# Kernel optimization log

Hardware: AMD Instinct MI355X
Metric: run time of the kernel (lower is better)

Reference implementation:

```python
import jax, jax.numpy as jnp
import numpy as np

EPS = 1e-5


def _interp_conv(x, pos_in, pos_out, idx, w1, b1, w2, b2, kernel, bias):
    # x: [B, Cin, Nin]; idx: [Nout, K] neighbor indices into the input grid.
    off = pos_in[idx] - pos_out[:, None, :]            # [Nout, K, 2] relative offsets
    h = jax.nn.relu(off @ w1 + b1)                     # [Nout, K, 16] weight-net hidden
    A = h @ w2 + b2                                    # [Nout, K, T] interp weights onto T kernel taps
    feat = x[:, :, idx]                                # [B, Cin, Nout, K] irregular gather
    taps = jnp.einsum('bcnk,nkt->bcnt', feat, A)       # resample neighbors onto canonical taps
    return jnp.einsum('bcnt,oct->bon', taps, kernel) + bias[None, :, None]


def _bn_relu(x, g, b):
    # BatchNorm1d (training-style batch stats over (B, N)) + ReLU
    m = x.mean(axis=(0, 2), keepdims=True)
    v = x.var(axis=(0, 2), keepdims=True)
    return jax.nn.relu((x - m) * jax.lax.rsqrt(v + EPS) * g[None, :, None] + b[None, :, None])


def setup_inputs():
    key = jax.random.key(0)
    ks = jax.random.split(key, 24)
    B, N1, N2, N3, K, T = 16, 50176, 12544, 3136, 9, 9
    d = {}
    d['x'] = jax.random.normal(ks[0], (B, 3, N1), jnp.float32)
    d['l1'] = jax.random.uniform(ks[1], (N1, 2), jnp.float32)
    d['l2'] = jax.random.uniform(ks[2], (N2, 2), jnp.float32)
    d['l3'] = jax.random.uniform(ks[3], (N3, 2), jnp.float32)
    d['knn1'] = jax.random.randint(ks[4], (N2, K), 0, N1)
    d['knn2'] = jax.random.randint(ks[5], (N2, K), 0, N2)
    d['knn3'] = jax.random.randint(ks[6], (N2, K), 0, N2)
    d['pool_idx'] = jax.random.randint(ks[7], (N3, 4), 0, N2)
    cins = {'c1': 3, 'c2': 32, 'c3': 32}
    couts = {'c1': 32, 'c2': 32, 'c3': 64}
    for i, p in enumerate(['c1', 'c2', 'c3']):
        d[p + '_wn_w1'] = jax.random.normal(ks[8 + 4 * i], (2, 16), jnp.float32) * 0.5
        d[p + '_wn_b1'] = jnp.zeros(16, jnp.float32)
        d[p + '_wn_w2'] = jax.random.normal(ks[9 + 4 * i], (16, T), jnp.float32) * 0.3
        d[p + '_wn_b2'] = jnp.zeros(T, jnp.float32)
        d[p + '_kernel'] = jax.random.normal(ks[10 + 4 * i], (couts[p], cins[p], T), jnp.float32) * np.float32(1.0 / np.sqrt(cins[p] * T))
        d[p + '_bias'] = jnp.zeros(couts[p], jnp.float32)
    for p, c in [('bn1', 32), ('bn2', 32), ('bn3', 64)]:
        d[p + '_g'] = jnp.ones(c, jnp.float32)
        d[p + '_b'] = jnp.zeros(c, jnp.float32)
    return d


def reference(x, l1, l2, l3, knn1, knn2, knn3, pool_idx,
              c1_wn_w1, c1_wn_b1, c1_wn_w2, c1_wn_b2, c1_kernel, c1_bias,
              c2_wn_w1, c2_wn_b1, c2_wn_w2, c2_wn_b2, c2_kernel, c2_bias,
              c3_wn_w1, c3_wn_b1, c3_wn_w2, c3_wn_b2, c3_kernel, c3_bias,
              bn1_g, bn1_b, bn2_g, bn2_b, bn3_g, bn3_b):
    h = _interp_conv(x, l1, l2, knn1, c1_wn_w1, c1_wn_b1, c1_wn_w2, c1_wn_b2, c1_kernel, c1_bias)
    h = _bn_relu(h, bn1_g, bn1_b)
    h = _interp_conv(h, l2, l2, knn2, c2_wn_w1, c2_wn_b1, c2_wn_w2, c2_wn_b2, c2_kernel, c2_bias)
    h = _bn_relu(h, bn2_g, bn2_b)
    h = _interp_conv(h, l2, l2, knn3, c3_wn_w1, c3_wn_b1, c3_wn_w2, c3_wn_b2, c3_kernel, c3_bias)
    h = _bn_relu(h, bn3_g, bn3_b)
    # MaxPoolNG: max over 4 nearest neighbors on the non-uniform grid -> [B, 64, N3]
    return h[:, :, pool_idx].max(axis=-1)
```

## Files before the change

### kernel.cpp

```cpp
#include <hip/hip_runtime.h>
#include <hip/hip_bf16.h>
#include <cfloat>

#define N1C 50176
#define N2C 12544
#define N3C 3136

typedef __attribute__((ext_vector_type(8))) short short8v;
typedef __attribute__((ext_vector_type(4))) float f32x4;

static __device__ __forceinline__ unsigned short f2bf(float f){
  __hip_bfloat16 h = __float2bfloat16(f);
  return *reinterpret_cast<unsigned short*>(&h);
}
static __device__ __forceinline__ float bflo(unsigned v){
  return __uint_as_float(v << 16);
}
static __device__ __forceinline__ float bfhi(unsigned v){
  return __uint_as_float(v & 0xFFFF0000u);
}
static __device__ __forceinline__ float bf2f(unsigned short u){
  return __uint_as_float(((unsigned)u) << 16);
}
static __device__ __forceinline__ unsigned pk2(float a, float b){
  return (unsigned)f2bf(a) | ((unsigned)f2bf(b) << 16);
}

__global__ __launch_bounds__(256) void transpose_x_kernel(
    const float* __restrict__ x, unsigned short* __restrict__ xTb)
{
  __shared__ float tile[48][65];
  int n0 = blockIdx.x * 64;
  int tid = threadIdx.x;
  int i = tid & 63;
  for (int rr = tid >> 6; rr < 48; rr += 4)
    tile[rr][i] = x[(size_t)rr * N1C + n0 + i];
  __syncthreads();
  for (int j = tid; j < 64*64; j += 256){
    int ii = j >> 6, bc = j & 63, b = bc >> 2, c = bc & 3;
    float v = (c < 3) ? tile[b*3 + c][ii] : 0.f;
    xTb[(size_t)n0 * 64 + j] = f2bf(v);
  }
}

__global__ __launch_bounds__(256) void compute_A_kernel(
    const float* __restrict__ pos_in, const float* __restrict__ pos_out,
    const int* __restrict__ idx,
    const float* __restrict__ w1, const float* __restrict__ b1,
    const float* __restrict__ w2, const float* __restrict__ b2,
    float* __restrict__ Abuf)
{
  int g = blockIdx.x * 256 + threadIdx.x;
  if (g >= N2C * 9) return;
  int n = g / 9;
  int p = idx[g];
  float o0 = pos_in[2*p]   - pos_out[2*n];
  float o1 = pos_in[2*p+1] - pos_out[2*n+1];
  float A[9];
  #pragma unroll
  for (int t = 0; t < 9; t++) A[t] = b2[t];
  #pragma unroll
  for (int j = 0; j < 16; j++){
    float h = fmaxf(fmaf(o0, w1[j], fmaf(o1, w1[16+j], b1[j])), 0.f);
    #pragma unroll
    for (int t = 0; t < 9; t++) A[t] = fmaf(h, w2[j*9 + t], A[t]);
  }
  #pragma unroll
  for (int t = 0; t < 9; t++) Abuf[(size_t)g*9 + t] = A[t];
}

__global__ __launch_bounds__(256) void wcvt_kernel(
    const float* __restrict__ W, unsigned short* __restrict__ Wb,
    int total, int K, int KW, int mode)
{
  int i = blockIdx.x * 256 + threadIdx.x;
  if (i >= total) return;
  int o = i / KW, r = i % KW;
  float v;
  if (mode == 0){
    v = (r < K) ? W[o*K + r] : 0.f;
  } else {
    int t = r >> 5, c = r & 31;
    v = W[o*288 + c*9 + t];
  }
  Wb[i] = f2bf(v);
}

template<int CIN, int CINP, int COUT, int NPB, bool AFFINE>
__global__ __launch_bounds__(256) void conv_mfma_kernel(
    const unsigned short* __restrict__ in, const int* __restrict__ idx,
    const float* __restrict__ Abuf, const unsigned short* __restrict__ Wb,
    const float* __restrict__ bias,
    const float* __restrict__ scale, const float* __restrict__ shift,
    unsigned short* __restrict__ out, float* __restrict__ gpart)
{
  constexpr int K    = CIN * 9;
  constexpr int KW   = (K < 32) ? 32 : K;
  constexpr int KROW = (K < 32) ? 48 : 296;
  constexpr int CHUNKS = KW / 32;
  constexpr int OT   = COUT / 16;
  constexpr int HP   = CINP / 2;
  constexpr int PPT  = 16 * HP;

  __shared__ alignas(16) unsigned short Tb[NPB * 16 * KROW];
  __shared__ float As[NPB * 81];
  __shared__ int   Ip[NPB * 9];
  __shared__ float Sw[4 * COUT];
  __shared__ float Sq[4 * COUT];

  int n0 = blockIdx.x * NPB;
  int tid = threadIdx.x;
  for (int i = tid; i < NPB*81; i += 256) As[i] = Abuf[(size_t)n0*81 + i];
  if (tid < NPB*9) Ip[tid] = idx[n0*9 + tid];
  for (int i = tid; i < 4*COUT; i += 256){ Sw[i] = 0.f; Sq[i] = 0.f; }
  if (K < 32){
    for (int i = tid; i < NPB*16*KROW/2; i += 256) ((unsigned*)Tb)[i] = 0u;
  }
  __syncthreads();

  for (int u = tid; u < NPB*PPT; u += 256){
    int ni = u / PPT, loc = u % PPT;
    int b = loc / HP, c2 = loc % HP;
    const float* As_n = As + ni*81;
    const int*   ip   = Ip + ni*9;
    float scx=1.f, shx=0.f, scy=1.f, shy=0.f;
    if (AFFINE){
      scx = scale[2*c2];   shx = shift[2*c2];
      scy = scale[2*c2+1]; shy = shift[2*c2+1];
    }
    float fx[9], fy[9];
    #pragma unroll
    for (int k = 0; k < 9; k++){
      unsigned v = *(const unsigned*)(in + ((size_t)ip[k]*16 + b)*CINP + 2*c2);
      float x0 = bflo(v), y0 = bfhi(v);
      if (AFFINE){
        x0 = fmaxf(fmaf(x0, scx, shx), 0.f);
        y0 = fmaxf(fmaf(y0, scy, shy), 0.f);
      }
      fx[k] = x0; fy[k] = y0;
    }
    unsigned short e[18];
    #pragma unroll
    for (int t = 0; t < 9; t++){
      float s0 = 0.f, s1 = 0.f;
      #pragma unroll
      for (int k = 0; k < 9; k++){
        float a = As_n[k*9 + t];
        s0 = fmaf(fx[k], a, s0);
        s1 = fmaf(fy[k], a, s1);
      }
      e[t] = f2bf(s0); e[9+t] = f2bf(s1);
    }
    unsigned* dst = (unsigned*)(Tb + (ni*16 + b)*KROW + 18*c2);
    #pragma unroll
    for (int j = 0; j < 9; j++) dst[j] = (unsigned)e[2*j] | ((unsigned)e[2*j+1] << 16);
  }
  __syncthreads();

  int w = tid >> 6, l = tid & 63, lr = l & 15, lg = l >> 4;
  float smr[4] = {0,0,0,0}, sqr[4] = {0,0,0,0};
  int oBase = 0;
  for (int wi = w; wi < NPB*OT; wi += 4){
    int ni = wi / OT, ot = wi % OT;
    oBase = 16*ot + 4*lg;
    f32x4 acc;
    #pragma unroll
    for (int r = 0; r < 4; r++) acc[r] = bias[oBase + r];
    const short8v* ap = (const short8v*)(Wb + (size_t)(16*ot + lr)*KW) + lg;
    const short8v* bp = (const short8v*)(Tb + (ni*16 + lr)*KROW) + lg;
    #pragma unroll
    for (int kk = 0; kk < CHUNKS; kk++)
      acc = __builtin_amdgcn_mfma_f32_16x16x32_bf16(ap[kk*4], bp[kk*4], acc, 0, 0, 0);
    ushort4 o4;
    o4.x = f2bf(acc[0]); o4.y = f2bf(acc[1]); o4.z = f2bf(acc[2]); o4.w = f2bf(acc[3]);
    *(ushort4*)(out + ((size_t)(n0 + ni)*16 + lr)*COUT + oBase) = o4;
    #pragma unroll
    for (int r = 0; r < 4; r++){
      smr[r] += acc[r];
      sqr[r] = fmaf(acc[r], acc[r], sqr[r]);
    }
  }
  #pragma unroll
  for (int m = 1; m < 16; m <<= 1){
    #pragma unroll
    for (int r = 0; r < 4; r++){
      smr[r] += __shfl_xor(smr[r], m);
      sqr[r] += __shfl_xor(sqr[r], m);
    }
  }
  if (lr == 0){
    #pragma unroll
    for (int r = 0; r < 4; r++){
      Sw[w*COUT + oBase + r] = smr[r];
      Sq[w*COUT + oBase + r] = sqr[r];
    }
  }
  __syncthreads();
  for (int o = tid; o < COUT; o += 256){
    float sm = Sw[o] + Sw[COUT + o] + Sw[2*COUT + o] + Sw[3*COUT + o];
    float sq = Sq[o] + Sq[COUT + o] + Sq[2*COUT + o] + Sq[3*COUT + o];
    gpart[(size_t)blockIdx.x * 2*COUT + o] = sm;
    gpart[(size_t)blockIdx.x * 2*COUT + COUT + o] = sq;
  }
}

template<int COUT>
__global__ __launch_bounds__(256, 4) void conv_wave_kernel(
    const unsigned short* __restrict__ in, const int* __restrict__ idx,
    const float* __restrict__ Abuf, const unsigned short* __restrict__ Wb,
    const float* __restrict__ bias,
    const float* __restrict__ scale, const float* __restrict__ shift,
    unsigned short* __restrict__ out, float* __restrict__ gpart)
{
  constexpr int NPB  = 4;
  constexpr int KROW = 296;
  constexpr int OT   = COUT / 16;

  __shared__ alignas(16) unsigned short Tb[NPB * 16 * KROW];
  __shared__ float Sw[4 * COUT];
  __shared__ float Sq[4 * COUT];

  int tid = threadIdx.x;
  int w = tid >> 6, l = tid & 63;
  int n0 = blockIdx.x * NPB;

  int nws = __builtin_amdgcn_readfirstlane(n0 + w);

  float areg[81];
  {
    const float* Ap = Abuf + (size_t)nws * 81;
    #pragma unroll
    for (int j = 0; j < 81; j++) areg[j] = Ap[j];
  }
  int ip[9];
  {
    const int* ipr = idx + nws * 9;
    #pragma unroll
    for (int k = 0; k < 9; k++) ip[k] = ipr[k];
  }

  int b = l & 15, cg = l >> 4;
  float4 scA = *(const float4*)(scale + cg*8);
  float4 scB = *(const float4*)(scale + cg*8 + 4);
  float4 shA = *(const float4*)(shift + cg*8);
  float4 shB = *(const float4*)(shift + cg*8 + 4);

  uint4 rv[9];
  #pragma unroll
  for (int k = 0; k < 9; k++){
    const unsigned short* rp = in + (size_t)ip[k]*512 + b*32 + cg*8;
    rv[k] = *(const uint4*)rp;
  }

  unsigned short* drow = Tb + (size_t)(w*16 + b)*KROW + cg*8;
  #pragma unroll
  for (int h = 0; h < 2; h++){
    f32x4 sc4, sh4;
    if (h == 0){
      sc4[0]=scA.x; sc4[1]=scA.y; sc4[2]=scA.z; sc4[3]=scA.w;
      sh4[0]=shA.x; sh4[1]=shA.y; sh4[2]=shA.z; sh4[3]=shA.w;
    } else {
      sc4[0]=scB.x; sc4[1]=scB.y; sc4[2]=scB.z; sc4[3]=scB.w;
      sh4[0]=shB.x; sh4[1]=shB.y; sh4[2]=shB.z; sh4[3]=shB.w;
    }
    f32x4 tv0={0,0,0,0}, tv1={0,0,0,0}, tv2={0,0,0,0}, tv3={0,0,0,0},
          tv4={0,0,0,0}, tv5={0,0,0,0}, tv6={0,0,0,0}, tv7={0,0,0,0},
          tv8={0,0,0,0};
    #pragma unroll
    for (int k = 0; k < 9; k++){
      unsigned u0 = (h == 0) ? rv[k].x : rv[k].z;
      unsigned u1 = (h == 0) ? rv[k].y : rv[k].w;
      f32x4 f;
      f[0] = bflo(u0); f[1] = bfhi(u0); f[2] = bflo(u1); f[3] = bfhi(u1);
      f = f * sc4 + sh4;
      f[0] = fmaxf(f[0], 0.f); f[1] = fmaxf(f[1], 0.f);
      f[2] = fmaxf(f[2], 0.f); f[3] = fmaxf(f[3], 0.f);
      tv0 += f * areg[k*9 + 0];
      tv1 += f * areg[k*9 + 1];
      tv2 += f * areg[k*9 + 2];
      tv3 += f * areg[k*9 + 3];
      tv4 += f * areg[k*9 + 4];
      tv5 += f * areg[k*9 + 5];
      tv6 += f * areg[k*9 + 6];
      tv7 += f * areg[k*9 + 7];
      tv8 += f * areg[k*9 + 8];
    }
    unsigned short* dh = drow + h*4;
    { uint2 o; o.x = pk2(tv0[0],tv0[1]); o.y = pk2(tv0[2],tv0[3]); *(uint2*)(dh + 0*32) = o; }
    { uint2 o; o.x = pk2(tv1[0],tv1[1]); o.y = pk2(tv1[2],tv1[3]); *(uint2*)(dh + 1*32) = o; }
    { uint2 o; o.x = pk2(tv2[0],tv2[1]); o.y = pk2(tv2[2],tv2[3]); *(uint2*)(dh + 2*32) = o; }
    { uint2 o; o.x = pk2(tv3[0],tv3[1]); o.y = pk2(tv3[2],tv3[3]); *(uint2*)(dh + 3*32) = o; }
    { uint2 o; o.x = pk2(tv4[0],tv4[1]); o.y = pk2(tv4[2],tv4[3]); *(uint2*)(dh + 4*32) = o; }
    { uint2 o; o.x = pk2(tv5[0],tv5[1]); o.y = pk2(tv5[2],tv5[3]); *(uint2*)(dh + 5*32) = o; }
    { uint2 o; o.x = pk2(tv6[0],tv6[1]); o.y = pk2(tv6[2],tv6[3]); *(uint2*)(dh + 6*32) = o; }
    { uint2 o; o.x = pk2(tv7[0],tv7[1]); o.y = pk2(tv7[2],tv7[3]); *(uint2*)(dh + 7*32) = o; }
    { uint2 o; o.x = pk2(tv8[0],tv8[1]); o.y = pk2(tv8[2],tv8[3]); *(uint2*)(dh + 8*32) = o; }
  }

  int lr = l & 15, lg = l >> 4;
  const short8v* bp = (const short8v*)(Tb + (size_t)(w*16 + lr)*KROW) + lg;
  #pragma unroll
  for (int ot = 0; ot < OT; ot++){
    int oBase = 16*ot + 4*lg;
    f32x4 a3;
    #pragma unroll
    for (int r = 0; r < 4; r++) a3[r] = bias[oBase + r];
    const short8v* ap = (const short8v*)(Wb + (size_t)(16*ot + lr)*288) + lg;
    #pragma unroll
    for (int kk = 0; kk < 9; kk++)
      a3 = __builtin_amdgcn_mfma_f32_16x16x32_bf16(ap[kk*4], bp[kk*4], a3, 0, 0, 0);
    ushort4 o4;
    o4.x = f2bf(a3[0]); o4.y = f2bf(a3[1]); o4.z = f2bf(a3[2]); o4.w = f2bf(a3[3]);
    *(ushort4*)(out + ((size_t)(n0 + w)*16 + lr)*COUT + oBase) = o4;

    float smr[4], sqr[4];
    #pragma unroll
    for (int r = 0; r < 4; r++){ smr[r] = a3[r]; sqr[r] = a3[r]*a3[r]; }
    #pragma unroll
    for (int m = 1; m < 16; m <<= 1){
      #pragma unroll
      for (int r = 0; r < 4; r++){
        smr[r] += __shfl_xor(smr[r], m);
        sqr[r] += __shfl_xor(sqr[r], m);
      }
    }
    if (lr == 0){
      #pragma unroll
      for (int r = 0; r < 4; r++){
        Sw[w*COUT + oBase + r] = smr[r];
        Sq[w*COUT + oBase + r] = sqr[r];
      }
    }
  }
  __syncthreads();
  for (int o = tid; o < COUT; o += 256){
    float sm = Sw[o] + Sw[COUT + o] + Sw[2*COUT + o] + Sw[3*COUT + o];
    float sq = Sq[o] + Sq[COUT + o] + Sq[2*COUT + o] + Sq[3*COUT + o];
    gpart[(size_t)blockIdx.x * 2*COUT + o] = sm;
    gpart[(size_t)blockIdx.x * 2*COUT + COUT + o] = sq;
  }
}

__global__ __launch_bounds__(256) void bn_finalize_kernel(
    const float* __restrict__ gpart, int NB, int C,
    const float* __restrict__ g, const float* __restrict__ bb,
    float* __restrict__ sc, float* __restrict__ sh, float invN)
{
  int c = blockIdx.x;
  float sm = 0.f, sq = 0.f;
  for (int i = threadIdx.x; i < NB; i += 256){
    sm += gpart[(size_t)i*2*C + c];
    sq += gpart[(size_t)i*2*C + C + c];
  }
  #pragma unroll
  for (int off = 32; off > 0; off >>= 1){
    sm += __shfl_down(sm, off);
    sq += __shfl_down(sq, off);
  }
  __shared__ float rs[8];
  int wd = threadIdx.x >> 6, ln = threadIdx.x & 63;
  if (ln == 0){ rs[wd] = sm; rs[4+wd] = sq; }
  __syncthreads();
  if (threadIdx.x == 0){
    float S = rs[0]+rs[1]+rs[2]+rs[3], Q = rs[4]+rs[5]+rs[6]+rs[7];
    float mean = S * invN;
    float var  = fmaxf(Q * invN - mean*mean, 0.f);
    float s = g[c] * rsqrtf(var + 1e-5f);
    sc[c] = s;
    sh[c] = bb[c] - mean * s;
  }
}

__global__ __launch_bounds__(256) void pool_kernel(
    const unsigned short* __restrict__ h3, const int* __restrict__ pidx,
    const float* __restrict__ sc, const float* __restrict__ sh,
    float* __restrict__ out)
{
  __shared__ float P[16][1024];
  int m0 = blockIdx.x * 16;
  int tid = threadIdx.x;
  for (int mi = 0; mi < 16; mi++){
    int m = m0 + mi;
    int p0 = pidx[m*4+0], p1 = pidx[m*4+1], p2 = pidx[m*4+2], p3 = pidx[m*4+3];
    #pragma unroll
    for (int q = 0; q < 4; q++){
      int bo = tid + q*256;
      int o = bo & 63;
      float s = sc[o], h = sh[o];
      float v0 = fmaf(bf2f(h3[(size_t)p0*1024 + bo]), s, h);
      float v1 = fmaf(bf2f(h3[(size_t)p1*1024 + bo]), s, h);
      float v2 = fmaf(bf2f(h3[(size_t)p2*1024 + bo]), s, h);
      float v3 = fmaf(bf2f(h3[(size_t)p3*1024 + bo]), s, h);
      P[mi][bo] = fmaxf(fmaxf(fmaxf(v0,v1), fmaxf(v2,v3)), 0.f);
    }
  }
  __syncthreads();
  #pragma unroll
  for (int w = 0; w < 4; w++){
    int r = tid + w*256;
    float* dst = out + (size_t)r*N3C + m0;
    #pragma unroll
    for (int mi = 0; mi < 16; mi++) dst[mi] = P[mi][r];
  }
}

extern "C" void kernel_launch(void* const* d_in, const int* in_sizes, int n_in,
                              void* d_out, int out_size, void* d_ws, size_t ws_size,
                              hipStream_t stream)
{
  const float* x    = (const float*)d_in[0];
  const float* l1   = (const float*)d_in[1];
  const float* l2   = (const float*)d_in[2];
  const int* knn1   = (const int*)d_in[4];
  const int* knn2   = (const int*)d_in[5];
  const int* knn3   = (const int*)d_in[6];
  const int* pidx   = (const int*)d_in[7];

  const float* c1_w1 = (const float*)d_in[8];
  const float* c1_b1 = (const float*)d_in[9];
  const float* c1_w2 = (const float*)d_in[10];
  const float* c1_b2 = (const float*)d_in[11];
  const float* c1_k  = (const float*)d_in[12];
  const float* c1_bs = (const float*)d_in[13];
  const float* c2_w1 = (const float*)d_in[14];
  const float* c2_b1 = (const float*)d_in[15];
  const float* c2_w2 = (const float*)d_in[16];
  const float* c2_b2 = (const float*)d_in[17];
  const float* c2_k  = (const float*)d_in[18];
  const float* c2_bs = (const float*)d_in[19];
  const float* c3_w1 = (const float*)d_in[20];
  const float* c3_b1 = (const float*)d_in[21];
  const float* c3_w2 = (const float*)d_in[22];
  const float* c3_b2 = (const float*)d_in[23];
  const float* c3_k  = (const float*)d_in[24];
  const float* c3_bs = (const float*)d_in[25];
  const float* bn1_g = (const float*)d_in[26];
  const float* bn1_b = (const float*)d_in[27];
  const float* bn2_g = (const float*)d_in[28];
  const float* bn2_b = (const float*)d_in[29];
  const float* bn3_g = (const float*)d_in[30];
  const float* bn3_b = (const float*)d_in[31];

  char* ws = (char*)d_ws;
  unsigned short* xTb = (unsigned short*)(ws + 0);
  unsigned short* h1  = (unsigned short*)(ws + 6422528);
  unsigned short* h2  = (unsigned short*)(ws + 19267584);
  unsigned short* h3  = (unsigned short*)(ws + 32112640);
  float* Abuf         = (float*)(ws + 57802752);
  float* gpart        = (float*)(ws + 61867008);
  unsigned short* wb1 = (unsigned short*)(ws + 65078272);
  unsigned short* wb2 = (unsigned short*)(ws + 65081344);
  unsigned short* wb3 = (unsigned short*)(ws + 65099776);
  float* sc1 = (float*)(ws + 65137664); float* sh1 = sc1 + 32;
  float* sc2 = sh1 + 32;                float* sh2 = sc2 + 32;
  float* sc3 = sh2 + 32;                float* sh3 = sc3 + 64;

  const float invN = 1.0f / (float)(N2C * 16);
  const int ablocks = (N2C * 9 + 255) / 256;

  transpose_x_kernel<<<N1C/64, 256, 0, stream>>>(x, xTb);
  wcvt_kernel<<<(32*32 + 255)/256, 256, 0, stream>>>(c1_k, wb1, 32*32, 27, 32, 0);
  wcvt_kernel<<<(32*288 + 255)/256, 256, 0, stream>>>(c2_k, wb2, 32*288, 288, 288, 1);
  wcvt_kernel<<<(64*288 + 255)/256, 256, 0, stream>>>(c3_k, wb3, 64*288, 288, 288, 1);

  compute_A_kernel<<<ablocks, 256, 0, stream>>>(l1, l2, knn1, c1_w1, c1_b1, c1_w2, c1_b2, Abuf);
  conv_mfma_kernel<3, 4, 32, 8, false><<<N2C/8, 256, 0, stream>>>(
      xTb, knn1, Abuf, wb1, c1_bs, nullptr, nullptr, h1, gpart);
  bn_finalize_kernel<<<32, 256, 0, stream>>>(gpart, N2C/8, 32, bn1_g, bn1_b, sc1, sh1, invN);

  compute_A_kernel<<<ablocks, 256, 0, stream>>>(l2, l2, knn2, c2_w1, c2_b1, c2_w2, c2_b2, Abuf);
  conv_wave_kernel<32><<<N2C/4, 256, 0, stream>>>(
      h1, knn2, Abuf, wb2, c2_bs, sc1, sh1, h2, gpart);
  bn_finalize_kernel<<<32, 256, 0, stream>>>(gpart, N2C/4, 32, bn2_g, bn2_b, sc2, sh2, invN);

  compute_A_kernel<<<ablocks, 256, 0, stream>>>(l2, l2, knn3, c3_w1, c3_b1, c3_w2, c3_b2, Abuf);
  conv_wave_kernel<64><<<N2C/4, 256, 0, stream>>>(
      h2, knn3, Abuf, wb3, c3_bs, sc2, sh2, h3, gpart);
  bn_finalize_kernel<<<64, 256, 0, stream>>>(gpart, N2C/4, 64, bn3_g, bn3_b, sc3, sh3, invN);

  pool_kernel<<<N3C/16, 256, 0, stream>>>(h3, pidx, sc3, sh3, (float*)d_out);
}
```

Baseline: 160.9 us.

## Split each conv point across two waves with 512-thread blocks

The wave-level conv kernel now uses two waves per output point instead of one. Each wave gathers and interpolates half of the 32 input channels into shared memory. After a block barrier, each wave runs the MFMA for half of the output tiles. This halves per-wave gather and FMA work and doubles the waves in flight to hide irregular gather latency. In exchange it adds a __syncthreads, loads the 81 A weights redundantly in both waves, and tightens launch bounds to 512x6, which may raise register pressure.

```diff
diff --git a/kernel.cpp b/kernel.cpp
--- a/kernel.cpp
+++ b/kernel.cpp
@@ -205,7 +205,7 @@
 }
 
 template<int COUT>
-__global__ __launch_bounds__(256, 4) void conv_wave_kernel(
+__global__ __launch_bounds__(512, 6) void conv_wave_kernel(
     const unsigned short* __restrict__ in, const int* __restrict__ idx,
     const float* __restrict__ Abuf, const unsigned short* __restrict__ Wb,
     const float* __restrict__ bias,
@@ -215,16 +215,18 @@
   constexpr int NPB  = 4;
   constexpr int KROW = 296;
   constexpr int OT   = COUT / 16;
+  constexpr int OTW  = OT / 2;
 
   __shared__ alignas(16) unsigned short Tb[NPB * 16 * KROW];
-  __shared__ float Sw[4 * COUT];
-  __shared__ float Sq[4 * COUT];
+  __shared__ float Sw[NPB * COUT];
+  __shared__ float Sq[NPB * COUT];
 
   int tid = threadIdx.x;
   int w = tid >> 6, l = tid & 63;
+  int pi = w >> 1, hf = w & 1;
   int n0 = blockIdx.x * NPB;
 
-  int nws = __builtin_amdgcn_readfirstlane(n0 + w);
+  int nws = __builtin_amdgcn_readfirstlane(n0 + pi);
 
   float areg[81];
   {
@@ -240,67 +242,58 @@
   }
 
   int b = l & 15, cg = l >> 4;
-  float4 scA = *(const float4*)(scale + cg*8);
-  float4 scB = *(const float4*)(scale + cg*8 + 4);
-  float4 shA = *(const float4*)(shift + cg*8);
-  float4 shB = *(const float4*)(shift + cg*8 + 4);
-
-  uint4 rv[9];
+  int ch0 = hf*16 + cg*4;
+  float4 scf = *(const float4*)(scale + ch0);
+  float4 shf = *(const float4*)(shift + ch0);
+  f32x4 sc4; sc4[0]=scf.x; sc4[1]=scf.y; sc4[2]=scf.z; sc4[3]=scf.w;
+  f32x4 sh4; sh4[0]=shf.x; sh4[1]=shf.y; sh4[2]=shf.z; sh4[3]=shf.w;
+
+  uint2 rv[9];
   #pragma unroll
   for (int k = 0; k < 9; k++){
-    const unsigned short* rp = in + (size_t)ip[k]*512 + b*32 + cg*8;
-    rv[k] = *(const uint4*)rp;
-  }
-
-  unsigned short* drow = Tb + (size_t)(w*16 + b)*KROW + cg*8;
-  #pragma unroll
-  for (int h = 0; h < 2; h++){
-    f32x4 sc4, sh4;
-    if (h == 0){
-      sc4[0]=scA.x; sc4[1]=scA.y; sc4[2]=scA.z; sc4[3]=scA.w;
-      sh4[0]=shA.x; sh4[1]=shA.y; sh4[2]=shA.z; sh4[3]=shA.w;
-    } else {
-      sc4[0]=scB.x; sc4[1]=scB.y; sc4[2]=scB.z; sc4[3]=scB.w;
-      sh4[0]=shB.x; sh4[1]=shB.y; sh4[2]=shB.z; sh4[3]=shB.w;
-    }
-    f32x4 tv0={0,0,0,0}, tv1={0,0,0,0}, tv2={0,0,0,0}, tv3={0,0,0,0},
-          tv4={0,0,0,0}, tv5={0,0,0,0}, tv6={0,0,0,0}, tv7={0,0,0,0},
-          tv8={0,0,0,0};
-    #pragma unroll
-    for (int k = 0; k < 9; k++){
-      unsigned u0 = (h == 0) ? rv[k].x : rv[k].z;
-      unsigned u1 = (h == 0) ? rv[k].y : rv[k].w;
-      f32x4 f;
-      f[0] = bflo(u0); f[1] = bfhi(u0); f[2] = bflo(u1); f[3] = bfhi(u1);
-      f = f * sc4 + sh4;
-      f[0] = fmaxf(f[0], 0.f); f[1] = fmaxf(f[1], 0.f);
-      f[2] = fmaxf(f[2], 0.f); f[3] = fmaxf(f[3], 0.f);
-      tv0 += f * areg[k*9 + 0];
-      tv1 += f * areg[k*9 + 1];
-      tv2 += f * areg[k*9 + 2];
-      tv3 += f * areg[k*9 + 3];
-      tv4 += f * areg[k*9 + 4];
-      tv5 += f * areg[k*9 + 5];
-      tv6 += f * areg[k*9 + 6];
-      tv7 += f * areg[k*9 + 7];
-      tv8 += f * areg[k*9 + 8];
-    }
-    unsigned short* dh = drow + h*4;
-    { uint2 o; o.x = pk2(tv0[0],tv0[1]); o.y = pk2(tv0[2],tv0[3]); *(uint2*)(dh + 0*32) = o; }
-    { uint2 o; o.x = pk2(tv1[0],tv1[1]); o.y = pk2(tv1[2],tv1[3]); *(uint2*)(dh + 1*32) = o; }
-    { uint2 o; o.x = pk2(tv2[0],tv2[1]); o.y = pk2(tv2[2],tv2[3]); *(uint2*)(dh + 2*32) = o; }
-    { uint2 o; o.x = pk2(tv3[0],tv3[1]); o.y = pk2(tv3[2],tv3[3]); *(uint2*)(dh + 3*32) = o; }
-    { uint2 o; o.x = pk2(tv4[0],tv4[1]); o.y = pk2(tv4[2],tv4[3]); *(uint2*)(dh + 4*32) = o; }
-    { uint2 o; o.x = pk2(tv5[0],tv5[1]); o.y = pk2(tv5[2],tv5[3]); *(uint2*)(dh + 5*32) = o; }
-    { uint2 o; o.x = pk2(tv6[0],tv6[1]); o.y = pk2(tv6[2],tv6[3]); *(uint2*)(dh + 6*32) = o; }
-    { uint2 o; o.x = pk2(tv7[0],tv7[1]); o.y = pk2(tv7[2],tv7[3]); *(uint2*)(dh + 7*32) = o; }
-    { uint2 o; o.x = pk2(tv8[0],tv8[1]); o.y = pk2(tv8[2],tv8[3]); *(uint2*)(dh + 8*32) = o; }
-  }
+    const unsigned short* rp = in + (size_t)ip[k]*512 + b*32 + ch0;
+    rv[k] = *(const uint2*)rp;
+  }
+
+  f32x4 tv0={0,0,0,0}, tv1={0,0,0,0}, tv2={0,0,0,0}, tv3={0,0,0,0},
+        tv4={0,0,0,0}, tv5={0,0,0,0}, tv6={0,0,0,0}, tv7={0,0,0,0},
+        tv8={0,0,0,0};
+  #pragma unroll
+  for (int k = 0; k < 9; k++){
+    unsigned u0 = rv[k].x, u1 = rv[k].y;
+    f32x4 f;
+    f[0] = bflo(u0); f[1] = bfhi(u0); f[2] = bflo(u1); f[3] = bfhi(u1);
+    f = f * sc4 + sh4;
+    f[0] = fmaxf(f[0], 0.f); f[1] = fmaxf(f[1], 0.f);
+    f[2] = fmaxf(f[2], 0.f); f[3] = fmaxf(f[3], 0.f);
+    tv0 += f * areg[k*9 + 0];
+    tv1 += f * areg[k*9 + 1];
+    tv2 += f * areg[k*9 + 2];
+    tv3 += f * areg[k*9 + 3];
+    tv4 += f * areg[k*9 + 4];
+    tv5 += f * areg[k*9 + 5];
+    tv6 += f * areg[k*9 + 6];
+    tv7 += f * areg[k*9 + 7];
+    tv8 += f * areg[k*9 + 8];
+  }
+  unsigned short* drow = Tb + (size_t)(pi*16 + b)*KROW + ch0;
+  { uint2 o; o.x = pk2(tv0[0],tv0[1]); o.y = pk2(tv0[2],tv0[3]); *(uint2*)(drow + 0*32) = o; }
+  { uint2 o; o.x = pk2(tv1[0],tv1[1]); o.y = pk2(tv1[2],tv1[3]); *(uint2*)(drow + 1*32) = o; }
+  { uint2 o; o.x = pk2(tv2[0],tv2[1]); o.y = pk2(tv2[2],tv2[3]); *(uint2*)(drow + 2*32) = o; }
+  { uint2 o; o.x = pk2(tv3[0],tv3[1]); o.y = pk2(tv3[2],tv3[3]); *(uint2*)(drow + 3*32) = o; }
+  { uint2 o; o.x = pk2(tv4[0],tv4[1]); o.y = pk2(tv4[2],tv4[3]); *(uint2*)(drow + 4*32) = o; }
+  { uint2 o; o.x = pk2(tv5[0],tv5[1]); o.y = pk2(tv5[2],tv5[3]); *(uint2*)(drow + 5*32) = o; }
+  { uint2 o; o.x = pk2(tv6[0],tv6[1]); o.y = pk2(tv6[2],tv6[3]); *(uint2*)(drow + 6*32) = o; }
+  { uint2 o; o.x = pk2(tv7[0],tv7[1]); o.y = pk2(tv7[2],tv7[3]); *(uint2*)(drow + 7*32) = o; }
+  { uint2 o; o.x = pk2(tv8[0],tv8[1]); o.y = pk2(tv8[2],tv8[3]); *(uint2*)(drow + 8*32) = o; }
+
+  __syncthreads();
 
   int lr = l & 15, lg = l >> 4;
-  const short8v* bp = (const short8v*)(Tb + (size_t)(w*16 + lr)*KROW) + lg;
-  #pragma unroll
-  for (int ot = 0; ot < OT; ot++){
+  const short8v* bp = (const short8v*)(Tb + (size_t)(pi*16 + lr)*KROW) + lg;
+  #pragma unroll
+  for (int oti = 0; oti < OTW; oti++){
+    int ot = hf*OTW + oti;
     int oBase = 16*ot + 4*lg;
     f32x4 a3;
     #pragma unroll
@@ -311,7 +304,7 @@
       a3 = __builtin_amdgcn_mfma_f32_16x16x32_bf16(ap[kk*4], bp[kk*4], a3, 0, 0, 0);
     ushort4 o4;
     o4.x = f2bf(a3[0]); o4.y = f2bf(a3[1]); o4.z = f2bf(a3[2]); o4.w = f2bf(a3[3]);
-    *(ushort4*)(out + ((size_t)(n0 + w)*16 + lr)*COUT + oBase) = o4;
+    *(ushort4*)(out + ((size_t)(n0 + pi)*16 + lr)*COUT + oBase) = o4;
 
     float smr[4], sqr[4];
     #pragma unroll
@@ -327,13 +320,13 @@
     if (lr == 0){
       #pragma unroll
       for (int r = 0; r < 4; r++){
-        Sw[w*COUT + oBase + r] = smr[r];
-        Sq[w*COUT + oBase + r] = sqr[r];
+        Sw[pi*COUT + oBase + r] = smr[r];
+        Sq[pi*COUT + oBase + r] = sqr[r];
       }
     }
   }
   __syncthreads();
-  for (int o = tid; o < COUT; o += 256){
+  for (int o = tid; o < COUT; o += 512){
     float sm = Sw[o] + Sw[COUT + o] + Sw[2*COUT + o] + Sw[3*COUT + o];
     float sq = Sq[o] + Sq[COUT + o] + Sq[2*COUT + o] + Sq[3*COUT + o];
     gpart[(size_t)blockIdx.x * 2*COUT + o] = sm;
@@ -469,12 +462,12 @@
   bn_finalize_kernel<<<32, 256, 0, stream>>>(gpart, N2C/8, 32, bn1_g, bn1_b, sc1, sh1, invN);
 
   compute_A_kernel<<<ablocks, 256, 0, stream>>>(l2, l2, knn2, c2_w1, c2_b1, c2_w2, c2_b2, Abuf);
-  conv_wave_kernel<32><<<N2C/4, 256, 0, stream>>>(
+  conv_wave_kernel<32><<<N2C/4, 512, 0, stream>>>(
       h1, knn2, Abuf, wb2, c2_bs, sc1, sh1, h2, gpart);
   bn_finalize_kernel<<<32, 256, 0, stream>>>(gpart, N2C/4, 32, bn2_g, bn2_b, sc2, sh2, invN);
 
   compute_A_kernel<<<ablocks, 256, 0, stream>>>(l2, l2, knn3, c3_w1, c3_b1, c3_w2, c3_b2, Abuf);
-  conv_wave_kernel<64><<<N2C/4, 256, 0, stream>>>(
+  conv_wave_kernel<64><<<N2C/4, 512, 0, stream>>>(
       h2, knn3, Abuf, wb3, c3_bs, sc2, sh2, h3, gpart);
   bn_finalize_kernel<<<64, 256, 0, stream>>>(gpart, N2C/4, 64, bn3_g, bn3_b, sc3, sh3, invN);
 
```

Measured after the change: 170.0 us. 1.06x slower.
